# Optimization experiments

Measured on AMD Instinct MI355X. Metric: run time of the kernel, lower is better.

The kernel has to match this reference:

```python
import jax, jax.numpy as jnp
import numpy as np
import math

B, C, N, M = 4, 128, 4096, 4096

def setup_inputs() -> dict:
    key = jax.random.key(0)
    ks = jax.random.split(key, 8)
    return {
        "x1": jax.random.normal(ks[0], (B, C, N), dtype=jnp.float32),
        "p1": jax.random.normal(ks[1], (B, 3, N), dtype=jnp.float32),
        "x2": jax.random.normal(ks[2], (B, C, M), dtype=jnp.float32),
        "p2": jax.random.normal(ks[3], (B, 3, M), dtype=jnp.float32),
        "Wq": jax.random.normal(ks[4], (C, C), dtype=jnp.float32) * 0.05,
        "Wk": jax.random.normal(ks[5], (C, C), dtype=jnp.float32) * 0.05,
        "Wv": jax.random.normal(ks[6], (C, C), dtype=jnp.float32) * 0.05,
        "Wpos": jax.random.normal(ks[7], (C, 3), dtype=jnp.float32) * 0.05,
    }

def reference(x1, p1, x2, p2, Wq, Wk, Wv, Wpos):
    # Conv1d with kernel_size=1, no bias == per-point matmul over channel dim.
    # NOTE: original forward uses self.pos for BOTH p1 and p2 (pos1 conv unused).
    pos = jnp.einsum('ck,bkn->bcn', Wpos, p1)   # [B,C,N]
    pos1 = jnp.einsum('ck,bkm->bcm', Wpos, p2)  # [B,C,M]
    q = jnp.einsum('dc,bcn->bdn', Wq, x1 + pos)   # [B,C,N]
    k = jnp.einsum('dc,bcm->bdm', Wk, x2 + pos1)  # [B,C,M]
    v = jnp.einsum('dc,bcm->bdm', Wv, x2)         # [B,C,M]
    scale = math.sqrt(q.shape[1])  # sqrt(C) -- q.shape[-2] in (B,C,N) layout
    energy = jnp.einsum('bcn,bcm->bnm', q, k) / scale  # [B,N,M]
    attention = jax.nn.softmax(energy, axis=-1)
    vout = jnp.einsum('bnm,bcm->bnc', attention, v)    # [B,N,C]
    out = jnp.swapaxes(vout, 1, 2) + x1                # [B,C,N] residual
    return jnp.swapaxes(out, 1, 2)                     # [B,N,C]
```

## Files before the change

### kernel.cpp

```cpp
#include <hip/hip_runtime.h>
#include <hip/hip_bf16.h>

#define B_ 4
#define C_ 128
#define N_ 4096
#define M_ 4096

typedef __bf16 bf16;
typedef __bf16 bf16x8 __attribute__((ext_vector_type(8)));
typedef float f32x4 __attribute__((ext_vector_type(4)));
typedef float f32x16 __attribute__((ext_vector_type(16)));

#define MFMA16(a, b, c) __builtin_amdgcn_mfma_f32_16x16x32_bf16(a, b, c, 0, 0, 0)
#define MFMA32(a, b, c) __builtin_amdgcn_mfma_f32_32x32x16_bf16(a, b, c, 0, 0, 0)

__device__ inline void gll16(const bf16* g, bf16* l) {
    __builtin_amdgcn_global_load_lds(
        (const __attribute__((address_space(1))) void*)g,
        (__attribute__((address_space(3))) void*)l, 16, 0, 0);
}

__device__ inline unsigned cvtpk(float a, float b) {
    unsigned r;
    asm("v_cvt_pk_bf16_f32 %0, %1, %2" : "=v"(r) : "v"(a), "v"(b));
    return r;
}

__global__ __launch_bounds__(256) void wcvt_kernel(
    const float* __restrict__ Wq, const float* __restrict__ Wk,
    const float* __restrict__ Wv, bf16* __restrict__ Wb) {
    int i = (blockIdx.x * 256 + threadIdx.x) * 4;
    const float* src = (i < 16384) ? Wq : (i < 32768) ? Wk : Wv;
    int off = i & 16383;
    float4 v = *(const float4*)(src + off);
    union { ushort4 u4; bf16 h[4]; } pk;
    pk.h[0] = (bf16)v.x; pk.h[1] = (bf16)v.y;
    pk.h[2] = (bf16)v.z; pk.h[3] = (bf16)v.w;
    *(ushort4*)(Wb + i) = pk.u4;
}

__global__ __launch_bounds__(768) void proj_kernel(
    const float* __restrict__ x1, const float* __restrict__ p1,
    const float* __restrict__ x2, const float* __restrict__ p2,
    const bf16* __restrict__ Wb, const float* __restrict__ Wpos,
    bf16* __restrict__ Qt, bf16* __restrict__ Kt, bf16* __restrict__ Vt) {
    __shared__ __align__(16) bf16 xp1[64 * 136];
    __shared__ __align__(16) bf16 xp2[64 * 136];
    __shared__ __align__(16) bf16 xr2[64 * 136];
    __shared__ float pp1[3 * 64], pp2[3 * 64], wls[384];

    const int t = threadIdx.x;
    const int b = blockIdx.y;
    const int n0 = blockIdx.x * 64;

    if (t < 48) {
        int k3 = t / 16, i4 = (t & 15) * 4;
        *(float4*)&pp1[k3 * 64 + i4] = *(const float4*)(p1 + ((size_t)b * 3 + k3) * N_ + n0 + i4);
    } else if (t < 96) {
        int tt = t - 48;
        int k3 = tt / 16, i4 = (tt & 15) * 4;
        *(float4*)&pp2[k3 * 64 + i4] = *(const float4*)(p2 + ((size_t)b * 3 + k3) * N_ + n0 + i4);
    } else if (t < 192) {
        int i4 = (t - 96) * 4;
        *(float4*)&wls[i4] = *(const float4*)(Wpos + i4);
    }
    __syncthreads();

    for (int s = t; s < 2048; s += 768) {
        int c = s >> 4, n4 = (s & 15) * 4;
        float4 xv = *(const float4*)(x1 + ((size_t)b * C_ + c) * N_ + n0 + n4);
        float w0 = wls[c * 3 + 0], w1 = wls[c * 3 + 1], w2 = wls[c * 3 + 2];
        const float* xa = &xv.x;
        #pragma unroll
        for (int j = 0; j < 4; ++j) {
            float pos = w0 * pp1[n4 + j] + w1 * pp1[64 + n4 + j] + w2 * pp1[128 + n4 + j];
            xp1[(n4 + j) * 136 + c] = (bf16)(xa[j] + pos);
        }
    }
    for (int s = t; s < 2048; s += 768) {
        int c = s >> 4, n4 = (s & 15) * 4;
        float4 xv = *(const float4*)(x2 + ((size_t)b * C_ + c) * N_ + n0 + n4);
        float w0 = wls[c * 3 + 0], w1 = wls[c * 3 + 1], w2 = wls[c * 3 + 2];
        const float* xa = &xv.x;
        #pragma unroll
        for (int j = 0; j < 4; ++j) {
            float pos = w0 * pp2[n4 + j] + w1 * pp2[64 + n4 + j] + w2 * pp2[128 + n4 + j];
            xp2[(n4 + j) * 136 + c] = (bf16)(xa[j] + pos);
            xr2[(n4 + j) * 136 + c] = (bf16)xa[j];
        }
    }
    __syncthreads();

    const int w = t >> 6;
    const int lane = t & 63;
    const int col = lane & 15, quad = lane >> 4;
    const int role = w >> 2, band = w & 3;
    const int nl = band * 16 + col;
    const int n = n0 + nl;

    const bf16* src = (role == 0) ? xp1 : (role == 1) ? xp2 : xr2;
    const bf16* Wm = Wb + role * 16384;

    bf16x8 bx[4];
    #pragma unroll
    for (int cs = 0; cs < 4; ++cs)
        bx[cs] = *(const bf16x8*)&src[nl * 136 + cs * 32 + quad * 8];

    #pragma unroll
    for (int dt = 0; dt < 8; ++dt) {
        f32x4 acc = {0.f, 0.f, 0.f, 0.f};
        #pragma unroll
        for (int cs = 0; cs < 4; ++cs) {
            bf16x8 wf = *(const bf16x8*)(Wm + (dt * 16 + col) * 128 + cs * 32 + quad * 8);
            acc = MFMA16(wf, bx[cs], acc);
        }
        if (role < 2) {
            bf16* Ot = (role == 0) ? Qt : Kt;
            union { ushort4 u4; bf16 h[4]; } pk;
            #pragma unroll
            for (int r = 0; r < 4; ++r) pk.h[r] = (bf16)acc[r];
            *(ushort4*)(Ot + ((size_t)b * N_ + n) * C_ + dt * 16 + quad * 4) = pk.u4;
        } else {
            #pragma unroll
            for (int r = 0; r < 4; ++r)
                Vt[((size_t)b * C_ + dt * 16 + quad * 4 + r) * (size_t)M_ + n] = (bf16)acc[r];
        }
    }
}

__global__ __launch_bounds__(512) void attn_kernel(
    const bf16* __restrict__ Qt, const bf16* __restrict__ Kt,
    const bf16* __restrict__ Vt, const float* __restrict__ x1,
    float* __restrict__ out) {
    __shared__ __align__(16) char smem[163840];

    const int t = threadIdx.x;
    const int w = t >> 6;
    const int lane = t & 63;
    const int col = lane & 31;
    const int hi = lane >> 5;
    const int kg = w & 3;
    const int qg = w >> 2;

    const int g0 = blockIdx.x;
    const int xcd = g0 & 7;
    const int b = xcd >> 1;
    const int qt = (xcd & 1) + ((g0 >> 3) << 1);
    const int n0 = qt * 64;

    const float KS = 0.12752107168406815f;

    const bf16* Kbase = Kt + (size_t)b * M_ * C_;
    const bf16* Vbase = Vt + (size_t)b * C_ * M_;

    bf16x8 qf[8];
    {
        const bf16* Qb = Qt + ((size_t)b * N_ + n0 + qg * 32 + col) * C_ + hi * 8;
        #pragma unroll
        for (int cs = 0; cs < 8; ++cs)
            qf[cs] = *(const bf16x8*)(Qb + cs * 16);
    }

    f32x16 oacc[4];
    #pragma unroll
    for (int i = 0; i < 4; ++i)
        #pragma unroll
        for (int j = 0; j < 16; ++j) oacc[i][j] = 0.f;
    float lacc = 0.f;

    const int key_l = (kg << 5) + col;
    const int kxor = (key_l & 15) << 4;

    auto stageK = [&](int m0, int dstOff) {
        #pragma unroll
        for (int i = 0; i < 4; ++i) {
            int g = ((w << 2) + i) * 64 + lane;
            int key = g >> 4;
            int sp = (g & 15) ^ (key & 15);
            gll16(Kbase + (size_t)(m0 + key) * C_ + sp * 8,
                  (bf16*)(smem + dstOff) + ((w << 2) + i) * 512);
        }
    };
    auto stageV = [&](int m0, int dstOff) {
        #pragma unroll
        for (int i = 0; i < 4; ++i) {
            int g = ((w << 2) + i) * 64 + lane;
            int c = g >> 4;
            int sp = (g & 15) ^ (c & 15);
            gll16(Vbase + (size_t)c * M_ + m0 + sp * 8,
                  (bf16*)(smem + dstOff) + ((w << 2) + i) * 512);
        }
    };

    stageK(0, 0);
    stageV(0, 98304);
    stageK(128, 32768);

    int koR = 0;
    int koW = 65536;
    int voR = 98304;

    for (int ch = 0; ch < 32; ++ch) {
        if (ch < 31) asm volatile("s_waitcnt vmcnt(4)" ::: "memory");
        else         asm volatile("s_waitcnt vmcnt(0)" ::: "memory");
        __builtin_amdgcn_sched_barrier(0);
        __builtin_amdgcn_s_barrier();
        __builtin_amdgcn_sched_barrier(0);

        if (ch < 31) stageV((ch + 1) << 7, voR ^ 32768);
        if (ch < 30) stageK((ch + 2) << 7, koW);

        const char* kbp = smem + koR + key_l * 256;

        f32x16 s0a, s1a;
        #pragma unroll
        for (int j = 0; j < 16; ++j) { s0a[j] = 0.f; s1a[j] = 0.f; }
        __builtin_amdgcn_s_setprio(1);
        #pragma unroll
        for (int cs = 0; cs < 4; ++cs) {
            bf16x8 kf = *(const bf16x8*)(kbp + ((((cs << 1) + hi) << 4) ^ kxor));
            s0a = MFMA32(kf, qf[cs], s0a);
        }
        #pragma unroll
        for (int cs = 4; cs < 8; ++cs) {
            bf16x8 kf = *(const bf16x8*)(kbp + ((((cs << 1) + hi) << 4) ^ kxor));
            s1a = MFMA32(kf, qf[cs], s1a);
        }
        __builtin_amdgcn_s_setprio(0);

        float p[16];
        #pragma unroll
        for (int r = 0; r < 16; ++r) {
            float e = fminf((s0a[r] + s1a[r]) * KS, 60.f);
            p[r] = __builtin_amdgcn_exp2f(e);
        }
        {
            float s01 = (p[0] + p[1]) + (p[2] + p[3]);
            float s23 = (p[4] + p[5]) + (p[6] + p[7]);
            float s45 = (p[8] + p[9]) + (p[10] + p[11]);
            float s67 = (p[12] + p[13]) + (p[14] + p[15]);
            lacc += (s01 + s23) + (s45 + s67);
        }
        unsigned W0 = cvtpk(p[0], p[1]),  W1 = cvtpk(p[2], p[3]);
        unsigned W2 = cvtpk(p[4], p[5]),  W3 = cvtpk(p[6], p[7]);
        unsigned W4 = cvtpk(p[8], p[9]),  W5 = cvtpk(p[10], p[11]);
        unsigned W6 = cvtpk(p[12], p[13]), W7 = cvtpk(p[14], p[15]);
        unsigned X0 = hi ? W0 : W2, X1 = hi ? W1 : W3;
        unsigned Y0 = hi ? W4 : W6, Y1 = hi ? W5 : W7;
        X0 = __shfl_xor(X0, 32, 64);  X1 = __shfl_xor(X1, 32, 64);
        Y0 = __shfl_xor(Y0, 32, 64);  Y1 = __shfl_xor(Y1, 32, 64);
        uint4 u0, u1;
        u0.x = hi ? X0 : W0;  u0.y = hi ? X1 : W1;
        u0.z = hi ? W2 : X0;  u0.w = hi ? W3 : X1;
        u1.x = hi ? Y0 : W4;  u1.y = hi ? Y1 : W5;
        u1.z = hi ? W6 : Y0;  u1.w = hi ? W7 : Y1;
        bf16x8 af0 = __builtin_bit_cast(bf16x8, u0);
        bf16x8 af1 = __builtin_bit_cast(bf16x8, u1);

        const char* vbB = smem + voR;
        __builtin_amdgcn_s_setprio(1);
        #pragma unroll
        for (int ct = 0; ct < 4; ++ct) {
            int c = (ct << 5) + col;
            const char* vbp = vbB + c * 256;
            int vxor = (c & 15) << 4;
            bf16x8 vf0 = *(const bf16x8*)(vbp + ((((kg << 2) + hi) << 4) ^ vxor));
            bf16x8 vf1 = *(const bf16x8*)(vbp + ((((kg << 2) + 2 + hi) << 4) ^ vxor));
            oacc[ct] = MFMA32(af0, vf0, oacc[ct]);
            oacc[ct] = MFMA32(af1, vf1, oacc[ct]);
        }
        __builtin_amdgcn_s_setprio(0);

        koR += 32768; if (koR == 98304) koR = 0;
        koW += 32768; if (koW == 98304) koW = 0;
        voR ^= 32768;
    }

    asm volatile("s_waitcnt lgkmcnt(0)" ::: "memory");
    __builtin_amdgcn_sched_barrier(0);
    __builtin_amdgcn_s_barrier();

    float* obuf = (float*)smem;
    float* lps  = (float*)(smem + 131072);

    lacc += __shfl_xor(lacc, 32, 64);
    if (hi == 0) lps[(kg << 6) + (qg << 5) + col] = lacc;

    #pragma unroll
    for (int ct = 0; ct < 4; ++ct)
        #pragma unroll
        for (int r = 0; r < 16; ++r) {
            int q = (r & 3) + ((r >> 2) << 3) + (hi << 2);
            obuf[kg * 8192 + ((qg << 5) + q) * 128 + (ct << 5) + col] = oacc[ct][r];
        }
    __syncthreads();

    const int c2 = lane << 1;
    #pragma unroll
    for (int j = 0; j < 8; ++j) {
        int q = (w << 3) + j;
        float s0 = 0.f, s1 = 0.f;
        #pragma unroll
        for (int pp = 0; pp < 4; ++pp) {
            float2 v = *(const float2*)&obuf[pp * 8192 + q * 128 + c2];
            s0 += v.x; s1 += v.y;
        }
        float lsum = lps[q] + lps[64 + q] + lps[128 + q] + lps[192 + q];
        float linv = 1.0f / lsum;
        int n = n0 + q;
        float o0 = s0 * linv + x1[((size_t)b * C_ + c2) * N_ + n];
        float o1 = s1 * linv + x1[((size_t)b * C_ + c2 + 1) * N_ + n];
        *(float2*)&out[((size_t)b * N_ + n) * C_ + c2] = make_float2(o0, o1);
    }
}

extern "C" void kernel_launch(void* const* d_in, const int* in_sizes, int n_in,
                              void* d_out, int out_size, void* d_ws, size_t ws_size,
                              hipStream_t stream) {
    const float* x1   = (const float*)d_in[0];
    const float* p1   = (const float*)d_in[1];
    const float* x2   = (const float*)d_in[2];
    const float* p2   = (const float*)d_in[3];
    const float* Wq   = (const float*)d_in[4];
    const float* Wk   = (const float*)d_in[5];
    const float* Wv   = (const float*)d_in[6];
    const float* Wpos = (const float*)d_in[7];
    float* out = (float*)d_out;

    bf16* Qt = (bf16*)d_ws;
    bf16* Kt = Qt + (size_t)B_ * N_ * C_;
    bf16* Vt = Kt + (size_t)B_ * M_ * C_;

    bf16* Wb = (bf16*)d_out;

    wcvt_kernel<<<dim3(48), dim3(256), 0, stream>>>(Wq, Wk, Wv, Wb);
    proj_kernel<<<dim3(64, B_), dim3(768), 0, stream>>>(
        x1, p1, x2, p2, Wb, Wpos, Qt, Kt, Vt);
    attn_kernel<<<dim3(256), dim3(512), 0, stream>>>(Qt, Kt, Vt, x1, out);
}
```

Baseline: 145.2 us.

## Software-pipeline QK^T one chunk ahead of softmax/PV with two K buffers

Restructures the attention main loop so the QK^T MFMAs for the next key chunk are issued before the softmax and PV of the current chunk, using a 2x-unrolled loop with ping-pong score registers. K staging drops from three LDS buffers to two, which shrinks shared memory. Global load addresses are precomputed once and advanced by pointer increments instead of being recomputed each stage. Waits are tightened to vmcnt(0) every half-iteration, which may expose load latency, and the extra live score accumulators raise register pressure.

After: 143.9 us. About the same (-0.9%).

```diff
diff --git a/kernel.cpp b/kernel.cpp
--- a/kernel.cpp
+++ b/kernel.cpp
@@ -132,7 +132,7 @@
     const bf16* __restrict__ Qt, const bf16* __restrict__ Kt,
     const bf16* __restrict__ Vt, const float* __restrict__ x1,
     float* __restrict__ out) {
-    __shared__ __align__(16) char smem[163840];
+    __shared__ __align__(16) char smem[132096];
 
     const int t = threadIdx.x;
     const int w = t >> 6;
@@ -171,67 +171,61 @@
     const int key_l = (kg << 5) + col;
     const int kxor = (key_l & 15) << 4;
 
-    auto stageK = [&](int m0, int dstOff) {
+    const bf16* kpp[4];
+    const bf16* vpp[4];
+    #pragma unroll
+    for (int i = 0; i < 4; ++i) {
+        int g = ((w << 2) + i) * 64 + lane;
+        int row = g >> 4;
+        int sp = (g & 15) ^ (row & 15);
+        kpp[i] = Kbase + (size_t)row * C_ + sp * 8;
+        vpp[i] = Vbase + (size_t)row * M_ + sp * 8;
+    }
+
+    auto stageK = [&](char* dst) {
         #pragma unroll
         for (int i = 0; i < 4; ++i) {
-            int g = ((w << 2) + i) * 64 + lane;
-            int key = g >> 4;
-            int sp = (g & 15) ^ (key & 15);
-            gll16(Kbase + (size_t)(m0 + key) * C_ + sp * 8,
-                  (bf16*)(smem + dstOff) + ((w << 2) + i) * 512);
+            gll16(kpp[i], (bf16*)dst + ((w << 2) + i) * 512);
+            kpp[i] += 128 * C_;
         }
     };
-    auto stageV = [&](int m0, int dstOff) {
+    auto stageV = [&](char* dst) {
         #pragma unroll
         for (int i = 0; i < 4; ++i) {
-            int g = ((w << 2) + i) * 64 + lane;
-            int c = g >> 4;
-            int sp = (g & 15) ^ (c & 15);
-            gll16(Vbase + (size_t)c * M_ + m0 + sp * 8,
-                  (bf16*)(smem + dstOff) + ((w << 2) + i) * 512);
+            gll16(vpp[i], (bf16*)dst + ((w << 2) + i) * 512);
+            vpp[i] += 128;
         }
     };
 
-    stageK(0, 0);
-    stageV(0, 98304);
-    stageK(128, 32768);
-
-    int koR = 0;
-    int koW = 65536;
-    int voR = 98304;
-
-    for (int ch = 0; ch < 32; ++ch) {
-        if (ch < 31) asm volatile("s_waitcnt vmcnt(4)" ::: "memory");
-        else         asm volatile("s_waitcnt vmcnt(0)" ::: "memory");
-        __builtin_amdgcn_sched_barrier(0);
-        __builtin_amdgcn_s_barrier();
-        __builtin_amdgcn_sched_barrier(0);
-
-        if (ch < 31) stageV((ch + 1) << 7, voR ^ 32768);
-        if (ch < 30) stageK((ch + 2) << 7, koW);
-
-        const char* kbp = smem + koR + key_l * 256;
-
-        f32x16 s0a, s1a;
-        #pragma unroll
-        for (int j = 0; j < 16; ++j) { s0a[j] = 0.f; s1a[j] = 0.f; }
+    stageK(smem);
+    stageV(smem + 65536);
+    stageK(smem + 32768);
+
+    f32x16 sA0, sA1, sB0, sB1;
+
+    auto qkc = [&](const char* kbBuf, f32x16& T0, f32x16& T1) {
+        #pragma unroll
+        for (int q = 0; q < 16; ++q) { T0[q] = 0.f; T1[q] = 0.f; }
+        const char* kbp = kbBuf + key_l * 256;
         __builtin_amdgcn_s_setprio(1);
         #pragma unroll
         for (int cs = 0; cs < 4; ++cs) {
             bf16x8 kf = *(const bf16x8*)(kbp + ((((cs << 1) + hi) << 4) ^ kxor));
-            s0a = MFMA32(kf, qf[cs], s0a);
+            T0 = MFMA32(kf, qf[cs], T0);
         }
         #pragma unroll
         for (int cs = 4; cs < 8; ++cs) {
             bf16x8 kf = *(const bf16x8*)(kbp + ((((cs << 1) + hi) << 4) ^ kxor));
-            s1a = MFMA32(kf, qf[cs], s1a);
+            T1 = MFMA32(kf, qf[cs], T1);
         }
         __builtin_amdgcn_s_setprio(0);
-
+    };
+
+    auto smpv = [&](f32x16& S0, f32x16& S1, const char* vbBuf) {
         float p[16];
         #pragma unroll
         for (int r = 0; r < 16; ++r) {
-            float e = fminf((s0a[r] + s1a[r]) * KS, 60.f);
+            float e = fminf((S0[r] + S1[r]) * KS, 60.f);
             p[r] = __builtin_amdgcn_exp2f(e);
         }
         {
@@ -257,12 +251,11 @@
         bf16x8 af0 = __builtin_bit_cast(bf16x8, u0);
         bf16x8 af1 = __builtin_bit_cast(bf16x8, u1);
 
-        const char* vbB = smem + voR;
         __builtin_amdgcn_s_setprio(1);
         #pragma unroll
         for (int ct = 0; ct < 4; ++ct) {
             int c = (ct << 5) + col;
-            const char* vbp = vbB + c * 256;
+            const char* vbp = vbBuf + c * 256;
             int vxor = (c & 15) << 4;
             bf16x8 vf0 = *(const bf16x8*)(vbp + ((((kg << 2) + hi) << 4) ^ vxor));
             bf16x8 vf1 = *(const bf16x8*)(vbp + ((((kg << 2) + 2 + hi) << 4) ^ vxor));
@@ -270,14 +263,40 @@
             oacc[ct] = MFMA32(af1, vf1, oacc[ct]);
         }
         __builtin_amdgcn_s_setprio(0);
-
-        koR += 32768; if (koR == 98304) koR = 0;
-        koW += 32768; if (koW == 98304) koW = 0;
-        voR ^= 32768;
-    }
-
-    asm volatile("s_waitcnt lgkmcnt(0)" ::: "memory");
+    };
+
+    asm volatile("s_waitcnt vmcnt(8)" ::: "memory");
     __builtin_amdgcn_sched_barrier(0);
+    __builtin_amdgcn_s_barrier();
+    __builtin_amdgcn_sched_barrier(0);
+    qkc(smem, sA0, sA1);
+
+    for (int jp = 0; jp < 16; ++jp) {
+        const int j0 = jp * 2, j1 = j0 + 1;
+
+        asm volatile("s_waitcnt vmcnt(0)" ::: "memory");
+        __builtin_amdgcn_sched_barrier(0);
+        __builtin_amdgcn_s_barrier();
+        __builtin_amdgcn_sched_barrier(0);
+        if (j0 < 31) stageV(smem + 98304);
+        if (j0 < 30) stageK(smem);
+        if (j0 < 31) qkc(smem + 32768, sB0, sB1);
+        smpv(sA0, sA1, smem + 65536);
+        asm volatile("s_waitcnt lgkmcnt(0)" ::: "memory");
+        __builtin_amdgcn_sched_barrier(0);
+
+        asm volatile("s_waitcnt vmcnt(0)" ::: "memory");
+        __builtin_amdgcn_sched_barrier(0);
+        __builtin_amdgcn_s_barrier();
+        __builtin_amdgcn_sched_barrier(0);
+        if (j1 < 31) stageV(smem + 65536);
+        if (j1 < 30) stageK(smem + 32768);
+        if (j1 < 31) qkc(smem, sA0, sA1);
+        smpv(sB0, sB1, smem + 98304);
+        asm volatile("s_waitcnt lgkmcnt(0)" ::: "memory");
+        __builtin_amdgcn_sched_barrier(0);
+    }
+
     __builtin_amdgcn_s_barrier();
 
     float* obuf = (float*)smem;
```
